# Optimization experiments

Hardware: AMD Instinct MI355X
Metric: run time of the kernel (lower is better)

The kernel has to match this reference:

```python
import jax, jax.numpy as jnp
import numpy as np

S, N_STEP, N_AGENT = 16, 91, 128
N_PL, N_PL_NODE, N_TL_STOP = 2048, 20, 64
STEP_CURRENT = 10
N_HIST = STEP_CURRENT + 1
N_FUT = N_STEP - N_HIST
N_TARGET, N_OTHER, N_MAP, N_TL = 16, 64, 512, 40
INF = jnp.float32(jnp.inf)


def rad2rot(yaw):
    # right-multiply convention: p_local = (p - ref) @ rot == R(yaw)^T (p - ref)
    c, s = jnp.cos(yaw), jnp.sin(yaw)
    return jnp.stack([jnp.stack([c, -s], -1), jnp.stack([s, c], -1)], -2)


def rad2local(rad, ref):
    d = rad - ref
    return jnp.arctan2(jnp.sin(d), jnp.cos(d))


def gather_t(x, idx):
    # per-scene fancy gather: x [S, A, ...], idx [S, ...] -> [S, *idx.shape[1:], ...]
    return jax.vmap(lambda xa, ia: xa[ia])(x, idx)


def _forward(agent_valid, agent_pos, agent_vel, agent_spd, agent_acc,
             agent_yaw_bbox, agent_yaw_rate, agent_type, agent_role,
             agent_size, agent_cmd, map_valid, map_type, map_pos, map_dir,
             tl_valid, tl_state, tl_pos, tl_dir):
    # --- target selection (training mode) ---
    w = agent_role.sum(-1).astype(jnp.float32) + agent_valid[:, STEP_CURRENT].astype(jnp.float32)
    _, tidx = jax.lax.top_k(w, N_TARGET)  # [S, T]

    ref_pos = gather_t(agent_pos[:, STEP_CURRENT], tidx)[:, :, None]  # [S,T,1,2]
    ref_yaw = gather_t(agent_yaw_bbox[:, STEP_CURRENT, :, 0], tidx)   # [S,T]
    ref_rot = rad2rot(ref_yaw)                                        # [S,T,2,2]
    ref_type = gather_t(agent_type, tidx)
    ref_role = gather_t(agent_role, tidx)

    def hist(x):  # [S, step, A, ...] -> [S, A, H, ...]
        return jnp.swapaxes(x[:, :N_HIST], 1, 2)

    def fut(x):   # [S, step, A, ...] -> [S, A, F, ...]
        return jnp.swapaxes(x[:, N_HIST:], 1, 2)

    # --- agent-centric target states ---
    tgt_valid = gather_t(hist(agent_valid), tidx)
    tgt_pos = jnp.matmul(gather_t(hist(agent_pos), tidx) - ref_pos, ref_rot)
    tgt_vel = jnp.matmul(gather_t(hist(agent_vel), tidx), ref_rot)
    tgt_spd = gather_t(hist(agent_spd), tidx)
    tgt_acc = gather_t(hist(agent_acc), tidx)
    tgt_yaw = rad2local(gather_t(hist(agent_yaw_bbox), tidx), ref_yaw[:, :, None, None])
    tgt_yr = gather_t(hist(agent_yaw_rate), tidx)
    tgt_size = gather_t(agent_size, tidx)

    # --- ground truth future ---
    gt_valid = gather_t(fut(agent_valid), tidx)
    gt_pos = jnp.matmul(gather_t(fut(agent_pos), tidx) - ref_pos, ref_rot)
    gt_vel = jnp.matmul(gather_t(fut(agent_vel), tidx), ref_rot)
    gt_spd = gather_t(fut(agent_spd), tidx)
    gt_yaw = rad2local(gather_t(fut(agent_yaw_bbox), tidx), ref_yaw[:, :, None, None])
    gt_cmd = gather_t(agent_cmd, tidx)

    # --- other agents: exclude target, topk nearest ---
    valid_hist = hist(agent_valid)  # [S,A,H]
    excl = jnp.arange(N_AGENT)[None, None, :] == tidx[:, :, None]  # [S,T,A]
    other_valid = valid_hist[:, None] & ~excl[..., None]           # [S,T,A,H]
    od = jnp.linalg.norm(agent_pos[:, STEP_CURRENT][:, None] - ref_pos, axis=-1)  # [S,T,A]
    od = jnp.where(other_valid[..., STEP_CURRENT], od, INF)
    neg_od, oidx = jax.lax.top_k(-od, N_OTHER)  # smallest distances
    odist = -neg_od

    def gather_o(x):  # x [S,A,...] -> [S,T,O,...] (gather along agent dim)
        extra = x.ndim - 2
        return jnp.take_along_axis(x[:, None], oidx.reshape(oidx.shape + (1,) * extra), axis=2)

    oth_valid = gather_o(valid_hist) & (odist[..., None] < 2000.0)
    rp = ref_pos[:, :, None]  # [S,T,1,1,2]
    rr = ref_rot[:, :, None]  # [S,T,1,2,2]
    oth_pos = jnp.matmul(gather_o(hist(agent_pos)) - rp, rr)
    oth_vel = jnp.matmul(gather_o(hist(agent_vel)), rr)
    oth_spd = gather_o(hist(agent_spd))
    oth_acc = gather_o(hist(agent_acc))
    oth_yaw = rad2local(gather_o(hist(agent_yaw_bbox)), ref_yaw[:, :, None, None, None])
    oth_yr = gather_o(hist(agent_yaw_rate))
    oth_type = gather_o(agent_type)
    oth_role = gather_o(agent_role)
    oth_size = gather_o(agent_size)

    # --- map: topk nearest polylines (by first node) ---
    md = jnp.linalg.norm(map_pos[:, None, :, 0] - ref_pos, axis=-1)  # [S,T,P]
    md = jnp.where(map_valid[:, None, :, 0], md, INF)
    neg_md, midx = jax.lax.top_k(-md, N_MAP)
    mdist = -neg_md
    m_valid = gather_t(map_valid, midx) & (mdist[..., None] < 3000.0)
    m_type = gather_t(map_type, midx)
    m_pos = jnp.matmul(gather_t(map_pos, midx) - rp, rr)
    m_dir = jnp.matmul(gather_t(map_dir, midx), rr)

    # --- traffic lights: per-step topk nearest ---
    tlv = tl_valid[:, :N_HIST]  # [S,H,L]
    tlp = tl_pos[:, :N_HIST]    # [S,H,L,2]
    td = jnp.linalg.norm(tlp[:, None] - ref_pos[:, :, :, None, :], axis=-1)  # [S,T,H,L]
    td = jnp.where(tlv[:, None], td, INF)
    neg_td, tlidx = jax.lax.top_k(-td, N_TL)  # [S,T,H,K]
    tdist = -neg_td

    def gather_tl(x):  # x [S,H,L,...] -> [S,T,H,K,...]
        extra = x.ndim - 3
        return jnp.take_along_axis(x[:, None], tlidx.reshape(tlidx.shape + (1,) * extra), axis=3)

    tl_valid_o = gather_tl(tlv) & (tdist < 2000.0)
    tl_state_o = gather_tl(tl_state[:, :N_HIST])
    tl_pos_o = jnp.matmul(gather_tl(tlp) - rp, rr)
    tl_dir_o = jnp.matmul(gather_tl(tl_dir[:, :N_HIST]), rr)

    floats = (ref_pos, ref_rot, tgt_pos, tgt_vel, tgt_spd, tgt_acc, tgt_yaw,
              tgt_yr, tgt_size, gt_pos, gt_vel, gt_spd, gt_yaw,
              oth_pos, oth_vel, oth_spd, oth_acc, oth_yaw, oth_yr, oth_size,
              m_pos, m_dir, tl_pos_o, tl_dir_o)
    bools = (tidx, ref_type, ref_role, tgt_valid, gt_valid, gt_cmd,
             oth_valid, oth_type, oth_role, m_valid, m_type, tl_valid_o, tl_state_o)
    return floats, bools


def setup_inputs() -> dict:
    key = jax.random.key(0)
    ks = jax.random.split(key, 20)
    f = lambda i, shape, sc=1.0: jax.random.normal(ks[i], shape, jnp.float32) * sc
    b = lambda i, shape, p=0.9: jax.random.bernoulli(ks[i], p, shape)
    return dict(
        agent_valid=b(0, (S, N_STEP, N_AGENT)),
        agent_pos=f(1, (S, N_STEP, N_AGENT, 2), 50.0),
        agent_vel=f(2, (S, N_STEP, N_AGENT, 2)),
        agent_spd=f(3, (S, N_STEP, N_AGENT, 1)),
        agent_acc=f(4, (S, N_STEP, N_AGENT, 1)),
        agent_yaw_bbox=f(5, (S, N_STEP, N_AGENT, 1)),
        agent_yaw_rate=f(6, (S, N_STEP, N_AGENT, 1)),
        agent_type=b(7, (S, N_AGENT, 3), 0.33),
        agent_role=b(8, (S, N_AGENT, 3), 0.1),
        agent_size=jax.random.uniform(ks[9], (S, N_AGENT, 3), jnp.float32, 1.0, 5.0),
        agent_cmd=b(10, (S, N_AGENT, 8), 0.125),
        map_valid=b(11, (S, N_PL, N_PL_NODE)),
        map_type=b(12, (S, N_PL, 11), 0.1),
        map_pos=f(13, (S, N_PL, N_PL_NODE, 2), 100.0),
        map_dir=f(14, (S, N_PL, N_PL_NODE, 2)),
        tl_valid=b(15, (S, N_STEP, N_TL_STOP)),
        tl_state=b(16, (S, N_STEP, N_TL_STOP, 5), 0.2),
        tl_pos=f(17, (S, N_STEP, N_TL_STOP, 2), 100.0),
        tl_dir=f(18, (S, N_STEP, N_TL_STOP, 2)),
    )


def reference(agent_valid, agent_pos, agent_vel, agent_spd, agent_acc,
              agent_yaw_bbox, agent_yaw_rate, agent_type, agent_role,
              agent_size, agent_cmd, map_valid, map_type, map_pos, map_dir,
              tl_valid, tl_state, tl_pos, tl_dir):
    floats, bools = _forward(agent_valid, agent_pos, agent_vel, agent_spd,
                             agent_acc, agent_yaw_bbox, agent_yaw_rate,
                             agent_type, agent_role, agent_size, agent_cmd,
                             map_valid, map_type, map_pos, map_dir,
                             tl_valid, tl_state, tl_pos, tl_dir)
    return floats + bools
```

## Files before the change

kernel.cpp:

```cpp
#include <hip/hip_runtime.h>
#include <hip/hip_bf16.h>
#include <math.h>

#define SS 16
#define NSTEP 91
#define NA 128
#define NPL 2048
#define NPLN 20
#define NTLS 64
#define SC 10
#define NH 11
#define NF 80
#define NT 16
#define NO 64
#define NM 512
#define NTL 40

#define OFF_REF_POS   0
#define OFF_REF_ROT   512
#define OFF_TGT_POS   1536
#define OFF_TGT_VEL   7168
#define OFF_TGT_SPD   12800
#define OFF_TGT_ACC   15616
#define OFF_TGT_YAW   18432
#define OFF_TGT_YR    21248
#define OFF_TGT_SIZE  24064
#define OFF_GT_POS    24832
#define OFF_GT_VEL    65792
#define OFF_GT_SPD    106752
#define OFF_GT_YAW    127232
#define OFF_OTH_POS   147712
#define OFF_OTH_VEL   508160
#define OFF_OTH_SPD   868608
#define OFF_OTH_ACC   1048832
#define OFF_OTH_YAW   1229056
#define OFF_OTH_YR    1409280
#define OFF_OTH_SIZE  1589504
#define OFF_M_POS     1638656
#define OFF_M_DIR     6881536
#define OFF_TL_POS    12124416
#define OFF_TL_DIR    12349696
#define OFF_TIDX      12574976
#define OFF_REF_TYPE  12575232
#define OFF_REF_ROLE  12576000
#define OFF_TGT_VALID 12576768
#define OFF_GT_VALID  12579584
#define OFF_GT_CMD    12600064
#define OFF_OTH_VALID 12602112
#define OFF_OTH_TYPE  12782336
#define OFF_OTH_ROLE  12831488
#define OFF_M_VALID   12880640
#define OFF_M_TYPE    15502080
#define OFF_TL_VALID  16943872
#define OFF_TL_STATE  17056512

__device__ __forceinline__ unsigned long long
dist_key(float px, float py, float rx, float ry, int idx, bool valid) {
    if (!valid) return 0x7FF0000000000000ull | (unsigned long long)(unsigned)idx;
    double dx = (double)px - (double)rx;
    double dy = (double)py - (double)ry;
    double d  = sqrt(__dadd_rn(__dmul_rn(dx, dx), __dmul_rn(dy, dy)));
    unsigned long long b = (unsigned long long)__double_as_longlong(d);
    return (b & ~2047ull) | (unsigned long long)(unsigned)idx;
}
__device__ __forceinline__ bool key_lt(unsigned long long kk, double thr) {
    double d = __longlong_as_double((long long)(kk & ~2047ull));
    return d < thr;
}

__global__ void k1_targets(const int* __restrict__ agent_valid,
                           const float* __restrict__ agent_pos,
                           const float* __restrict__ agent_yaw,
                           const int* __restrict__ agent_type,
                           const int* __restrict__ agent_role,
                           const float* __restrict__ agent_size,
                           const int* __restrict__ agent_cmd,
                           float* __restrict__ out,
                           int* __restrict__ tidx_ws,
                           float* __restrict__ refx_ws,
                           float* __restrict__ refy_ws,
                           float* __restrict__ refyaw_ws) {
    __shared__ int wred[2];
    int s = blockIdx.x;
    int a = threadIdx.x;
    int w = agent_role[(s * NA + a) * 3 + 0] +
            agent_role[(s * NA + a) * 3 + 1] +
            agent_role[(s * NA + a) * 3 + 2] +
            agent_valid[(s * NSTEP + SC) * NA + a];
    int packed = (w << 8) | (127 - a);
    for (int p = 0; p < NT; ++p) {
        int v = packed;
        for (int d = 32; d > 0; d >>= 1) v = max(v, __shfl_xor(v, d));
        if ((threadIdx.x & 63) == 0) wred[threadIdx.x >> 6] = v;
        __syncthreads();
        int m = max(wred[0], wred[1]);
        __syncthreads();
        int best = 127 - (m & 0xFF);
        if (a == best) {
            packed = -1;
            int st = s * NT + p;
            tidx_ws[st] = a;
            out[OFF_TIDX + st] = (float)a;
            float px = agent_pos[((s * NSTEP + SC) * NA + a) * 2 + 0];
            float py = agent_pos[((s * NSTEP + SC) * NA + a) * 2 + 1];
            float yaw = agent_yaw[(s * NSTEP + SC) * NA + a];
            refx_ws[st] = px; refy_ws[st] = py; refyaw_ws[st] = yaw;
            float c = cosf(yaw), sn = sinf(yaw);
            out[OFF_REF_POS + st * 2 + 0] = px;
            out[OFF_REF_POS + st * 2 + 1] = py;
            out[OFF_REF_ROT + st * 4 + 0] = c;
            out[OFF_REF_ROT + st * 4 + 1] = -sn;
            out[OFF_REF_ROT + st * 4 + 2] = sn;
            out[OFF_REF_ROT + st * 4 + 3] = c;
            for (int k = 0; k < 3; ++k) {
                out[OFF_REF_TYPE + st * 3 + k] = (float)agent_type[(s * NA + a) * 3 + k];
                out[OFF_REF_ROLE + st * 3 + k] = (float)agent_role[(s * NA + a) * 3 + k];
                out[OFF_TGT_SIZE + st * 3 + k] = agent_size[(s * NA + a) * 3 + k];
            }
            for (int k = 0; k < 8; ++k)
                out[OFF_GT_CMD + st * 8 + k] = (float)agent_cmd[(s * NA + a) * 8 + k];
        }
    }
}

__global__ void k2_tgt(const int* __restrict__ agent_valid,
                       const float* __restrict__ agent_pos,
                       const float* __restrict__ agent_vel,
                       const float* __restrict__ agent_spd,
                       const float* __restrict__ agent_acc,
                       const float* __restrict__ agent_yaw,
                       const float* __restrict__ agent_yr,
                       float* __restrict__ out,
                       const int* __restrict__ tidx_ws,
                       const float* __restrict__ refx_ws,
                       const float* __restrict__ refy_ws,
                       const float* __restrict__ refyaw_ws) {
    int idx = blockIdx.x * blockDim.x + threadIdx.x;
    if (idx >= SS * NT * NSTEP) return;
    int step = idx % NSTEP;
    int t = (idx / NSTEP) % NT;
    int s = idx / (NSTEP * NT);
    int st = s * NT + t;
    int a = tidx_ws[st];
    float rx = refx_ws[st], ry = refy_ws[st], ryaw = refyaw_ws[st];
    float c = cosf(ryaw), sn = sinf(ryaw);
    int gi = (s * NSTEP + step) * NA + a;
    float2 p = *(const float2*)&agent_pos[gi * 2];
    float px = p.x - rx, py = p.y - ry;
    float2 v = *(const float2*)&agent_vel[gi * 2];
    float2 op = make_float2(px * c + py * sn, -px * sn + py * c);
    float2 ov = make_float2(v.x * c + v.y * sn, -v.x * sn + v.y * c);
    float spd = agent_spd[gi];
    float dyaw = agent_yaw[gi] - ryaw;
    float lyaw = atan2f(sinf(dyaw), cosf(dyaw));
    float vld = (float)agent_valid[gi];
    if (step < NH) {
        int hi = st * NH + step;
        *(float2*)&out[OFF_TGT_POS + hi * 2] = op;
        *(float2*)&out[OFF_TGT_VEL + hi * 2] = ov;
        out[OFF_TGT_SPD + hi] = spd;
        out[OFF_TGT_ACC + hi] = agent_acc[gi];
        out[OFF_TGT_YAW + hi] = lyaw;
        out[OFF_TGT_YR + hi] = agent_yr[gi];
        out[OFF_TGT_VALID + hi] = vld;
    } else {
        int fi = st * NF + (step - NH);
        *(float2*)&out[OFF_GT_POS + fi * 2] = op;
        *(float2*)&out[OFF_GT_VEL + fi * 2] = ov;
        out[OFF_GT_SPD + fi] = spd;
        out[OFF_GT_YAW + fi] = lyaw;
        out[OFF_GT_VALID + fi] = vld;
    }
}

__global__ void k3_others(const int* __restrict__ agent_valid,
                          const float* __restrict__ agent_pos,
                          const float* __restrict__ agent_vel,
                          const float* __restrict__ agent_spd,
                          const float* __restrict__ agent_acc,
                          const float* __restrict__ agent_yaw,
                          const float* __restrict__ agent_yr,
                          const int* __restrict__ agent_type,
                          const int* __restrict__ agent_role,
                          const float* __restrict__ agent_size,
                          float* __restrict__ out,
                          const int* __restrict__ tidx_ws,
                          const float* __restrict__ refx_ws,
                          const float* __restrict__ refy_ws,
                          const float* __restrict__ refyaw_ws) {
    __shared__ unsigned long long key[NA];
    int bid = blockIdx.x;
    int s = bid & (SS - 1), t = bid >> 4;
    int st = s * NT + t;
    int tid = threadIdx.x;
    float rx = refx_ws[st], ry = refy_ws[st], ryaw = refyaw_ws[st];
    float c = cosf(ryaw), sn = sinf(ryaw);
    int tgt = tidx_ws[st];
    {
        int a = tid;
        int va = agent_valid[(s * NSTEP + SC) * NA + a];
        float2 p = *(const float2*)&agent_pos[((s * NSTEP + SC) * NA + a) * 2];
        key[a] = dist_key(p.x, p.y, rx, ry, a, va && (a != tgt));
    }
    for (int k = 2; k <= NA; k <<= 1)
        for (int j = k >> 1; j > 0; j >>= 1) {
            __syncthreads();
            int i = tid, ixj = i ^ j;
            if (ixj > i) {
                unsigned long long x = key[i], y = key[ixj];
                bool up = ((i & k) == 0);
                if (up ? (x > y) : (x < y)) { key[i] = y; key[ixj] = x; }
            }
        }
    __syncthreads();
    if (tid < NO) {
        int o = tid;
        int oa = (int)(key[o] & 2047ull);
        int base = (st * NO + o) * 3;
        for (int k = 0; k < 3; ++k) {
            out[OFF_OTH_TYPE + base + k] = (float)agent_type[(s * NA + oa) * 3 + k];
            out[OFF_OTH_ROLE + base + k] = (float)agent_role[(s * NA + oa) * 3 + k];
            out[OFF_OTH_SIZE + base + k] = agent_size[(s * NA + oa) * 3 + k];
        }
    }
    for (int i = tid; i < NO * NH; i += blockDim.x) {
        int o = i / NH, h = i % NH;
        unsigned long long kk = key[o];
        int oa = (int)(kk & 2047ull);
        bool dok = key_lt(kk, 2000.0);
        int gi = (s * NSTEP + h) * NA + oa;
        int hi = (st * NO + o) * NH + h;
        float2 p = *(const float2*)&agent_pos[gi * 2];
        float px = p.x - rx, py = p.y - ry;
        *(float2*)&out[OFF_OTH_POS + hi * 2] = make_float2(px * c + py * sn, -px * sn + py * c);
        float2 v = *(const float2*)&agent_vel[gi * 2];
        *(float2*)&out[OFF_OTH_VEL + hi * 2] = make_float2(v.x * c + v.y * sn, -v.x * sn + v.y * c);
        out[OFF_OTH_SPD + hi] = agent_spd[gi];
        out[OFF_OTH_ACC + hi] = agent_acc[gi];
        float dyaw = agent_yaw[gi] - ryaw;
        out[OFF_OTH_YAW + hi] = atan2f(sinf(dyaw), cosf(dyaw));
        out[OFF_OTH_YR + hi] = agent_yr[gi];
        out[OFF_OTH_VALID + hi] = (agent_valid[gi] && dok) ? 1.0f : 0.0f;
    }
}

__global__ void __launch_bounds__(1024)
k4_map(const int* __restrict__ map_valid,
       const int* __restrict__ map_type,
       const float* __restrict__ map_pos,
       const float* __restrict__ map_dir,
       float* __restrict__ out,
       const float* __restrict__ refx_ws,
       const float* __restrict__ refy_ws,
       const float* __restrict__ refyaw_ws) {
    __shared__ unsigned long long key[NPL];
    int bid = blockIdx.x;
    int s = bid & (SS - 1), t = bid >> 4;
    int st = s * NT + t;
    int tid = threadIdx.x;
    float rx = refx_ws[st], ry = refy_ws[st], ryaw = refyaw_ws[st];
    float c = cosf(ryaw), sn = sinf(ryaw);
    #pragma unroll
    for (int e = 0; e < 2; ++e) {
        int pl = 2 * tid + e;
        int v0 = map_valid[(s * NPL + pl) * NPLN + 0];
        float2 p = *(const float2*)&map_pos[((s * NPL + pl) * NPLN + 0) * 2];
        key[pl] = dist_key(p.x, p.y, rx, ry, pl, v0 != 0);
    }
    for (int k = 2; k <= NPL; k <<= 1)
        for (int j = k >> 1; j > 0; j >>= 1) {
            __syncthreads();
            int i = ((tid & ~(j - 1)) << 1) | (tid & (j - 1));
            int pp = i | j;
            bool up = ((i & k) == 0);
            unsigned long long x = key[i], y = key[pp];
            if (up ? (x > y) : (x < y)) { key[i] = y; key[pp] = x; }
        }
    __syncthreads();
    for (int i = tid; i < NM * (NPLN / 2); i += 1024) {
        int r = i / (NPLN / 2), q = i % (NPLN / 2);
        int nd = 2 * q;
        unsigned long long kk = key[r];
        int pl = (int)(kk & 2047ull);
        bool dok = key_lt(kk, 3000.0);
        int gi = (s * NPL + pl) * NPLN + nd;
        int oi = (st * NM + r) * NPLN + nd;
        int2 mv = *(const int2*)&map_valid[gi];
        *(float2*)&out[OFF_M_VALID + oi] =
            make_float2((mv.x && dok) ? 1.0f : 0.0f, (mv.y && dok) ? 1.0f : 0.0f);
        float4 p = *(const float4*)&map_pos[gi * 2];
        float ax = p.x - rx, ay = p.y - ry;
        float bx = p.z - rx, by = p.w - ry;
        *(float4*)&out[OFF_M_POS + oi * 2] =
            make_float4(ax * c + ay * sn, -ax * sn + ay * c,
                        bx * c + by * sn, -bx * sn + by * c);
        float4 dd = *(const float4*)&map_dir[gi * 2];
        *(float4*)&out[OFF_M_DIR + oi * 2] =
            make_float4(dd.x * c + dd.y * sn, -dd.x * sn + dd.y * c,
                        dd.z * c + dd.w * sn, -dd.z * sn + dd.w * c);
    }
    for (int i = tid; i < NM * 11; i += 1024) {
        int r = i / 11, k = i % 11;
        int pl = (int)(key[r] & 2047ull);
        out[OFF_M_TYPE + (st * NM + r) * 11 + k] = (float)map_type[(s * NPL + pl) * 11 + k];
    }
}

__global__ void k5_tl(const int* __restrict__ tl_valid,
                      const int* __restrict__ tl_state,
                      const float* __restrict__ tl_pos,
                      const float* __restrict__ tl_dir,
                      float* __restrict__ out,
                      const float* __restrict__ refx_ws,
                      const float* __restrict__ refy_ws,
                      const float* __restrict__ refyaw_ws) {
    __shared__ unsigned long long key[NTLS];
    int bid = blockIdx.x;
    int h = bid % NH;
    int t = (bid / NH) % NT;
    int s = bid / (NH * NT);
    int st = s * NT + t;
    int tid = threadIdx.x;
    float rx = refx_ws[st], ry = refy_ws[st], ryaw = refyaw_ws[st];
    float c = cosf(ryaw), sn = sinf(ryaw);
    {
        int stop = tid;
        int va = tl_valid[(s * NSTEP + h) * NTLS + stop];
        float2 p = *(const float2*)&tl_pos[((s * NSTEP + h) * NTLS + stop) * 2];
        key[stop] = dist_key(p.x, p.y, rx, ry, stop, va != 0);
    }
    for (int k = 2; k <= NTLS; k <<= 1)
        for (int j = k >> 1; j > 0; j >>= 1) {
            __syncthreads();
            int i = tid, ixj = i ^ j;
            if (ixj > i) {
                unsigned long long x = key[i], y = key[ixj];
                bool up = ((i & k) == 0);
                if (up ? (x > y) : (x < y)) { key[i] = y; key[ixj] = x; }
            }
        }
    __syncthreads();
    if (tid < NTL) {
        int r = tid;
        unsigned long long kk = key[r];
        int stop = (int)(kk & 2047ull);
        bool dok = key_lt(kk, 2000.0);
        int gi = (s * NSTEP + h) * NTLS + stop;
        int oi = (st * NH + h) * NTL + r;
        out[OFF_TL_VALID + oi] = (tl_valid[gi] && dok) ? 1.0f : 0.0f;
        for (int k = 0; k < 5; ++k)
            out[OFF_TL_STATE + oi * 5 + k] = (float)tl_state[gi * 5 + k];
        float2 p = *(const float2*)&tl_pos[gi * 2];
        float px = p.x - rx, py = p.y - ry;
        *(float2*)&out[OFF_TL_POS + oi * 2] = make_float2(px * c + py * sn, -px * sn + py * c);
        float2 dd = *(const float2*)&tl_dir[gi * 2];
        *(float2*)&out[OFF_TL_DIR + oi * 2] = make_float2(dd.x * c + dd.y * sn, -dd.x * sn + dd.y * c);
    }
}

extern "C" void kernel_launch(void* const* d_in, const int* in_sizes, int n_in,
                              void* d_out, int out_size, void* d_ws, size_t ws_size,
                              hipStream_t stream) {
    const int*   agent_valid = (const int*)d_in[0];
    const float* agent_pos   = (const float*)d_in[1];
    const float* agent_vel   = (const float*)d_in[2];
    const float* agent_spd   = (const float*)d_in[3];
    const float* agent_acc   = (const float*)d_in[4];
    const float* agent_yaw   = (const float*)d_in[5];
    const float* agent_yr    = (const float*)d_in[6];
    const int*   agent_type  = (const int*)d_in[7];
    const int*   agent_role  = (const int*)d_in[8];
    const float* agent_size  = (const float*)d_in[9];
    const int*   agent_cmd   = (const int*)d_in[10];
    const int*   map_valid   = (const int*)d_in[11];
    const int*   map_type    = (const int*)d_in[12];
    const float* map_pos     = (const float*)d_in[13];
    const float* map_dir     = (const float*)d_in[14];
    const int*   tl_valid    = (const int*)d_in[15];
    const int*   tl_state    = (const int*)d_in[16];
    const float* tl_pos      = (const float*)d_in[17];
    const float* tl_dir      = (const float*)d_in[18];
    float* out = (float*)d_out;

    int*   tidx_ws   = (int*)d_ws;
    float* refx_ws   = (float*)((char*)d_ws + 1024);
    float* refy_ws   = (float*)((char*)d_ws + 2048);
    float* refyaw_ws = (float*)((char*)d_ws + 3072);

    hipLaunchKernelGGL(k1_targets, dim3(SS), dim3(NA), 0, stream,
                       agent_valid, agent_pos, agent_yaw, agent_type, agent_role,
                       agent_size, agent_cmd, out, tidx_ws, refx_ws, refy_ws, refyaw_ws);

    int n2 = SS * NT * NSTEP;
    hipLaunchKernelGGL(k2_tgt, dim3((n2 + 255) / 256), dim3(256), 0, stream,
                       agent_valid, agent_pos, agent_vel, agent_spd, agent_acc,
                       agent_yaw, agent_yr, out, tidx_ws, refx_ws, refy_ws, refyaw_ws);

    hipLaunchKernelGGL(k3_others, dim3(SS * NT), dim3(NA), 0, stream,
                       agent_valid, agent_pos, agent_vel, agent_spd, agent_acc,
                       agent_yaw, agent_yr, agent_type, agent_role, agent_size,
                       out, tidx_ws, refx_ws, refy_ws, refyaw_ws);

    hipLaunchKernelGGL(k4_map, dim3(SS * NT), dim3(1024), 0, stream,
                       map_valid, map_type, map_pos, map_dir, out,
                       refx_ws, refy_ws, refyaw_ws);

    hipLaunchKernelGGL(k5_tl, dim3(SS * NT * NH), dim3(NTLS), 0, stream,
                       tl_valid, tl_state, tl_pos, tl_dir, out,
                       refx_ws, refy_ws, refyaw_ws);
}
```

Measured before the change: 193.4 us.

## Split others/map kernels into sort-select and wide gather phases

The map and other-agent kernels are each split into a selection kernel, which sorts the distance keys and writes compact 16-bit indices with a validity bit to workspace, and a gather kernel that spreads the output writes over 8x (map) or 4x (others) more blocks. Previously the heavy map output gather ran in only 256 blocks, each stuck behind its own bitonic sort. The new layout should give many more waves for the memory-bound writes. In k1, the per-target output writes now happen in parallel after the top-k loop instead of serially inside it. The cost is extra kernel launches and a small workspace round trip.

Result: faster. 188.4 us (-2.6%).

```diff
diff --git a/kernel.cpp b/kernel.cpp
--- a/kernel.cpp
+++ b/kernel.cpp
@@ -54,6 +54,7 @@
 #define OFF_TL_VALID  16943872
 #define OFF_TL_STATE  17056512
 
+
 __device__ __forceinline__ unsigned long long
 dist_key(float px, float py, float rx, float ry, int idx, bool valid) {
     if (!valid) return 0x7FF0000000000000ull | (unsigned long long)(unsigned)idx;
@@ -81,6 +82,7 @@
                            float* __restrict__ refy_ws,
                            float* __restrict__ refyaw_ws) {
     __shared__ int wred[2];
+    __shared__ int bests[NT];
     int s = blockIdx.x;
     int a = threadIdx.x;
     int w = agent_role[(s * NA + a) * 3 + 0] +
@@ -96,30 +98,34 @@
         int m = max(wred[0], wred[1]);
         __syncthreads();
         int best = 127 - (m & 0xFF);
-        if (a == best) {
-            packed = -1;
-            int st = s * NT + p;
-            tidx_ws[st] = a;
-            out[OFF_TIDX + st] = (float)a;
-            float px = agent_pos[((s * NSTEP + SC) * NA + a) * 2 + 0];
-            float py = agent_pos[((s * NSTEP + SC) * NA + a) * 2 + 1];
-            float yaw = agent_yaw[(s * NSTEP + SC) * NA + a];
-            refx_ws[st] = px; refy_ws[st] = py; refyaw_ws[st] = yaw;
-            float c = cosf(yaw), sn = sinf(yaw);
-            out[OFF_REF_POS + st * 2 + 0] = px;
-            out[OFF_REF_POS + st * 2 + 1] = py;
-            out[OFF_REF_ROT + st * 4 + 0] = c;
-            out[OFF_REF_ROT + st * 4 + 1] = -sn;
-            out[OFF_REF_ROT + st * 4 + 2] = sn;
-            out[OFF_REF_ROT + st * 4 + 3] = c;
-            for (int k = 0; k < 3; ++k) {
-                out[OFF_REF_TYPE + st * 3 + k] = (float)agent_type[(s * NA + a) * 3 + k];
-                out[OFF_REF_ROLE + st * 3 + k] = (float)agent_role[(s * NA + a) * 3 + k];
-                out[OFF_TGT_SIZE + st * 3 + k] = agent_size[(s * NA + a) * 3 + k];
-            }
-            for (int k = 0; k < 8; ++k)
-                out[OFF_GT_CMD + st * 8 + k] = (float)agent_cmd[(s * NA + a) * 8 + k];
+        if (a == best) packed = -1;
+        if (threadIdx.x == 0) bests[p] = best;
+    }
+    __syncthreads();
+    if (a < NT) {
+        int p = a;
+        int ag = bests[p];
+        int st = s * NT + p;
+        tidx_ws[st] = ag;
+        out[OFF_TIDX + st] = (float)ag;
+        float px = agent_pos[((s * NSTEP + SC) * NA + ag) * 2 + 0];
+        float py = agent_pos[((s * NSTEP + SC) * NA + ag) * 2 + 1];
+        float yaw = agent_yaw[(s * NSTEP + SC) * NA + ag];
+        refx_ws[st] = px; refy_ws[st] = py; refyaw_ws[st] = yaw;
+        float c = cosf(yaw), sn = sinf(yaw);
+        out[OFF_REF_POS + st * 2 + 0] = px;
+        out[OFF_REF_POS + st * 2 + 1] = py;
+        out[OFF_REF_ROT + st * 4 + 0] = c;
+        out[OFF_REF_ROT + st * 4 + 1] = -sn;
+        out[OFF_REF_ROT + st * 4 + 2] = sn;
+        out[OFF_REF_ROT + st * 4 + 3] = c;
+        for (int k = 0; k < 3; ++k) {
+            out[OFF_REF_TYPE + st * 3 + k] = (float)agent_type[(s * NA + ag) * 3 + k];
+            out[OFF_REF_ROLE + st * 3 + k] = (float)agent_role[(s * NA + ag) * 3 + k];
+            out[OFF_TGT_SIZE + st * 3 + k] = agent_size[(s * NA + ag) * 3 + k];
         }
+        for (int k = 0; k < 8; ++k)
+            out[OFF_GT_CMD + st * 8 + k] = (float)agent_cmd[(s * NA + ag) * 8 + k];
     }
 }
 
@@ -173,28 +179,18 @@
     }
 }
 
-__global__ void k3_others(const int* __restrict__ agent_valid,
-                          const float* __restrict__ agent_pos,
-                          const float* __restrict__ agent_vel,
-                          const float* __restrict__ agent_spd,
-                          const float* __restrict__ agent_acc,
-                          const float* __restrict__ agent_yaw,
-                          const float* __restrict__ agent_yr,
-                          const int* __restrict__ agent_type,
-                          const int* __restrict__ agent_role,
-                          const float* __restrict__ agent_size,
-                          float* __restrict__ out,
-                          const int* __restrict__ tidx_ws,
-                          const float* __restrict__ refx_ws,
-                          const float* __restrict__ refy_ws,
-                          const float* __restrict__ refyaw_ws) {
+__global__ void k3a_sel(const int* __restrict__ agent_valid,
+                        const float* __restrict__ agent_pos,
+                        unsigned short* __restrict__ sel_ws,
+                        const int* __restrict__ tidx_ws,
+                        const float* __restrict__ refx_ws,
+                        const float* __restrict__ refy_ws) {
     __shared__ unsigned long long key[NA];
     int bid = blockIdx.x;
     int s = bid & (SS - 1), t = bid >> 4;
     int st = s * NT + t;
     int tid = threadIdx.x;
-    float rx = refx_ws[st], ry = refy_ws[st], ryaw = refyaw_ws[st];
-    float c = cosf(ryaw), sn = sinf(ryaw);
+    float rx = refx_ws[st], ry = refy_ws[st];
     int tgt = tidx_ws[st];
     {
         int a = tid;
@@ -214,20 +210,43 @@
         }
     __syncthreads();
     if (tid < NO) {
-        int o = tid;
-        int oa = (int)(key[o] & 2047ull);
-        int base = (st * NO + o) * 3;
-        for (int k = 0; k < 3; ++k) {
-            out[OFF_OTH_TYPE + base + k] = (float)agent_type[(s * NA + oa) * 3 + k];
-            out[OFF_OTH_ROLE + base + k] = (float)agent_role[(s * NA + oa) * 3 + k];
-            out[OFF_OTH_SIZE + base + k] = agent_size[(s * NA + oa) * 3 + k];
-        }
-    }
-    for (int i = tid; i < NO * NH; i += blockDim.x) {
-        int o = i / NH, h = i % NH;
-        unsigned long long kk = key[o];
-        int oa = (int)(kk & 2047ull);
-        bool dok = key_lt(kk, 2000.0);
+        unsigned long long kk = key[tid];
+        sel_ws[st * NO + tid] =
+            (unsigned short)((unsigned)(kk & 2047ull) | (key_lt(kk, 2000.0) ? 0x8000u : 0u));
+    }
+}
+
+__global__ void k3b_gather(const int* __restrict__ agent_valid,
+                           const float* __restrict__ agent_pos,
+                           const float* __restrict__ agent_vel,
+                           const float* __restrict__ agent_spd,
+                           const float* __restrict__ agent_acc,
+                           const float* __restrict__ agent_yaw,
+                           const float* __restrict__ agent_yr,
+                           const int* __restrict__ agent_type,
+                           const int* __restrict__ agent_role,
+                           const float* __restrict__ agent_size,
+                           float* __restrict__ out,
+                           const unsigned short* __restrict__ sel_ws,
+                           const float* __restrict__ refx_ws,
+                           const float* __restrict__ refy_ws,
+                           const float* __restrict__ refyaw_ws) {
+    __shared__ unsigned short sel[NO];
+    int bid = blockIdx.x;
+    int idx4 = bid >> 2, quarter = bid & 3;
+    int s = idx4 & (SS - 1), t = idx4 >> 4;
+    int st = s * NT + t;
+    int tid = threadIdx.x;
+    if (tid < NO) sel[tid] = sel_ws[st * NO + tid];
+    __syncthreads();
+    float rx = refx_ws[st], ry = refy_ws[st], ryaw = refyaw_ws[st];
+    float c = cosf(ryaw), sn = sinf(ryaw);
+    if (tid < 176) {
+        int item = quarter * 176 + tid;
+        int o = item / NH, h = item % NH;
+        unsigned short sv = sel[o];
+        int oa = sv & 2047;
+        bool dok = (sv & 0x8000u) != 0;
         int gi = (s * NSTEP + h) * NA + oa;
         int hi = (st * NO + o) * NH + h;
         float2 p = *(const float2*)&agent_pos[gi * 2];
@@ -242,24 +261,30 @@
         out[OFF_OTH_YR + hi] = agent_yr[gi];
         out[OFF_OTH_VALID + hi] = (agent_valid[gi] && dok) ? 1.0f : 0.0f;
     }
+    if (quarter == 0 && tid >= 192 && tid < 192 + NO) {
+        int o = tid - 192;
+        int oa = sel[o] & 2047;
+        int base = (st * NO + o) * 3;
+        for (int k = 0; k < 3; ++k) {
+            out[OFF_OTH_TYPE + base + k] = (float)agent_type[(s * NA + oa) * 3 + k];
+            out[OFF_OTH_ROLE + base + k] = (float)agent_role[(s * NA + oa) * 3 + k];
+            out[OFF_OTH_SIZE + base + k] = agent_size[(s * NA + oa) * 3 + k];
+        }
+    }
 }
 
 __global__ void __launch_bounds__(1024)
-k4_map(const int* __restrict__ map_valid,
-       const int* __restrict__ map_type,
-       const float* __restrict__ map_pos,
-       const float* __restrict__ map_dir,
-       float* __restrict__ out,
-       const float* __restrict__ refx_ws,
-       const float* __restrict__ refy_ws,
-       const float* __restrict__ refyaw_ws) {
+k4a_sel(const int* __restrict__ map_valid,
+        const float* __restrict__ map_pos,
+        unsigned short* __restrict__ sel_ws,
+        const float* __restrict__ refx_ws,
+        const float* __restrict__ refy_ws) {
     __shared__ unsigned long long key[NPL];
     int bid = blockIdx.x;
     int s = bid & (SS - 1), t = bid >> 4;
     int st = s * NT + t;
     int tid = threadIdx.x;
-    float rx = refx_ws[st], ry = refy_ws[st], ryaw = refyaw_ws[st];
-    float c = cosf(ryaw), sn = sinf(ryaw);
+    float rx = refx_ws[st], ry = refy_ws[st];
     #pragma unroll
     for (int e = 0; e < 2; ++e) {
         int pl = 2 * tid + e;
@@ -277,12 +302,40 @@
             if (up ? (x > y) : (x < y)) { key[i] = y; key[pp] = x; }
         }
     __syncthreads();
-    for (int i = tid; i < NM * (NPLN / 2); i += 1024) {
-        int r = i / (NPLN / 2), q = i % (NPLN / 2);
+    if (tid < NM) {
+        unsigned long long kk = key[tid];
+        sel_ws[st * NM + tid] =
+            (unsigned short)((unsigned)(kk & 2047ull) | (key_lt(kk, 3000.0) ? 0x8000u : 0u));
+    }
+}
+
+__global__ void k4b_gather(const int* __restrict__ map_valid,
+                           const int* __restrict__ map_type,
+                           const float* __restrict__ map_pos,
+                           const float* __restrict__ map_dir,
+                           float* __restrict__ out,
+                           const unsigned short* __restrict__ sel_ws,
+                           const float* __restrict__ refx_ws,
+                           const float* __restrict__ refy_ws,
+                           const float* __restrict__ refyaw_ws) {
+    __shared__ unsigned short sel[NM];
+    int bid = blockIdx.x;
+    int idx8 = bid >> 3, oct = bid & 7;
+    int s = idx8 & (SS - 1), t = idx8 >> 4;
+    int st = s * NT + t;
+    int tid = threadIdx.x;
+    sel[tid] = sel_ws[st * NM + tid];
+    sel[tid + 256] = sel_ws[st * NM + tid + 256];
+    __syncthreads();
+    float rx = refx_ws[st], ry = refy_ws[st], ryaw = refyaw_ws[st];
+    float c = cosf(ryaw), sn = sinf(ryaw);
+    for (int ii = tid; ii < 640; ii += 256) {
+        int item = oct * 640 + ii;
+        int r = item / (NPLN / 2), q = item % (NPLN / 2);
         int nd = 2 * q;
-        unsigned long long kk = key[r];
-        int pl = (int)(kk & 2047ull);
-        bool dok = key_lt(kk, 3000.0);
+        unsigned short sv = sel[r];
+        int pl = sv & 2047;
+        bool dok = (sv & 0x8000u) != 0;
         int gi = (s * NPL + pl) * NPLN + nd;
         int oi = (st * NM + r) * NPLN + nd;
         int2 mv = *(const int2*)&map_valid[gi];
@@ -299,9 +352,10 @@
             make_float4(dd.x * c + dd.y * sn, -dd.x * sn + dd.y * c,
                         dd.z * c + dd.w * sn, -dd.z * sn + dd.w * c);
     }
-    for (int i = tid; i < NM * 11; i += 1024) {
-        int r = i / 11, k = i % 11;
-        int pl = (int)(key[r] & 2047ull);
+    for (int ii = tid; ii < 704; ii += 256) {
+        int item = oct * 704 + ii;
+        int r = item / 11, k = item % 11;
+        int pl = sel[r] & 2047;
         out[OFF_M_TYPE + (st * NM + r) * 11 + k] = (float)map_type[(s * NPL + pl) * 11 + k];
     }
 }
@@ -386,24 +440,32 @@
     float* refx_ws   = (float*)((char*)d_ws + 1024);
     float* refy_ws   = (float*)((char*)d_ws + 2048);
     float* refyaw_ws = (float*)((char*)d_ws + 3072);
+    unsigned short* k3sel = (unsigned short*)((char*)d_ws + 4096);
+    unsigned short* k4sel = (unsigned short*)((char*)d_ws + 36864);
 
     hipLaunchKernelGGL(k1_targets, dim3(SS), dim3(NA), 0, stream,
                        agent_valid, agent_pos, agent_yaw, agent_type, agent_role,
                        agent_size, agent_cmd, out, tidx_ws, refx_ws, refy_ws, refyaw_ws);
+
+    hipLaunchKernelGGL(k4a_sel, dim3(SS * NT), dim3(1024), 0, stream,
+                       map_valid, map_pos, k4sel, refx_ws, refy_ws);
+
+    hipLaunchKernelGGL(k3a_sel, dim3(SS * NT), dim3(NA), 0, stream,
+                       agent_valid, agent_pos, k3sel, tidx_ws, refx_ws, refy_ws);
 
     int n2 = SS * NT * NSTEP;
     hipLaunchKernelGGL(k2_tgt, dim3((n2 + 255) / 256), dim3(256), 0, stream,
                        agent_valid, agent_pos, agent_vel, agent_spd, agent_acc,
                        agent_yaw, agent_yr, out, tidx_ws, refx_ws, refy_ws, refyaw_ws);
 
-    hipLaunchKernelGGL(k3_others, dim3(SS * NT), dim3(NA), 0, stream,
+    hipLaunchKernelGGL(k4b_gather, dim3(SS * NT * 8), dim3(256), 0, stream,
+                       map_valid, map_type, map_pos, map_dir, out,
+                       k4sel, refx_ws, refy_ws, refyaw_ws);
+
+    hipLaunchKernelGGL(k3b_gather, dim3(SS * NT * 4), dim3(256), 0, stream,
                        agent_valid, agent_pos, agent_vel, agent_spd, agent_acc,
                        agent_yaw, agent_yr, agent_type, agent_role, agent_size,
-                       out, tidx_ws, refx_ws, refy_ws, refyaw_ws);
-
-    hipLaunchKernelGGL(k4_map, dim3(SS * NT), dim3(1024), 0, stream,
-                       map_valid, map_type, map_pos, map_dir, out,
-                       refx_ws, refy_ws, refyaw_ws);
+                       out, k3sel, refx_ws, refy_ws, refyaw_ws);
 
     hipLaunchKernelGGL(k5_tl, dim3(SS * NT * NH), dim3(NTLS), 0, stream,
                        tl_valid, tl_state, tl_pos, tl_dir, out,
```
